# Performance work log

Measured on AMD Instinct MI355X. Metric: run time of the kernel, lower is better.

Reference implementation:

```python
import jax, jax.numpy as jnp
import numpy as np

B, S, D, H = 2, 2048, 1024, 16
HD = D // H
FF = 4 * D
EPS = 1e-5


def _ln(x, g, b):
    mu = jnp.mean(x, axis=-1, keepdims=True)
    var = jnp.var(x, axis=-1, keepdims=True)
    return (x - mu) * jax.lax.rsqrt(var + EPS) * g + b


def setup_inputs() -> dict:
    key = jax.random.key(0)
    ks = jax.random.split(key, 8)
    std = 0.02
    inp = {
        'x': jax.random.normal(ks[0], (B, S, D), jnp.float32),
        'mask': jnp.ones((B, S), jnp.int32),
        'Wq': jax.random.normal(ks[1], (D, D), jnp.float32) * std,
        'bq': jnp.zeros((D,), jnp.float32),
        'Wk': jax.random.normal(ks[2], (D, D), jnp.float32) * std,
        'bk': jnp.zeros((D,), jnp.float32),
        'Wv': jax.random.normal(ks[3], (D, D), jnp.float32) * std,
        'bv': jnp.zeros((D,), jnp.float32),
        'Wo': jax.random.normal(ks[4], (D, D), jnp.float32) * std,
        'bo': jnp.zeros((D,), jnp.float32),
        'W1': jax.random.normal(ks[5], (D, FF), jnp.float32) * std,
        'b1': jnp.zeros((FF,), jnp.float32),
        'W2': jax.random.normal(ks[6], (FF, D), jnp.float32) * std,
        'b2': jnp.zeros((D,), jnp.float32),
        'g1': jnp.ones((D,), jnp.float32),
        'be1': jnp.zeros((D,), jnp.float32),
        'g2': jnp.ones((D,), jnp.float32),
        'be2': jnp.zeros((D,), jnp.float32),
    }
    return inp


def reference(x, mask, Wq, bq, Wk, bk, Wv, bv, Wo, bo, W1, b1, W2, b2, g1, be1, g2, be2):
    # multi-head attention (dropout in eval mode => identity)
    q = (x @ Wq + bq).reshape(B, S, H, HD).transpose(0, 2, 1, 3)  # [B,H,S,HD]
    k = (x @ Wk + bk).reshape(B, S, H, HD).transpose(0, 2, 1, 3)
    v = (x @ Wv + bv).reshape(B, S, H, HD).transpose(0, 2, 1, 3)
    scores = jnp.einsum('bhqd,bhkd->bhqk', q, k) / jnp.sqrt(jnp.float32(HD))
    m = mask[:, None, None, :]  # [B,1,1,S] broadcast over queries
    scores = jnp.where(m == 0, jnp.float32(-1e9), scores)
    attn = jax.nn.softmax(scores, axis=-1)
    ao = jnp.einsum('bhqk,bhkd->bhqd', attn, v).transpose(0, 2, 1, 3).reshape(B, S, D)
    attn_out = ao @ Wo + bo
    x1 = _ln(x + attn_out, g1, be1)
    ffn = jax.nn.relu(x1 @ W1 + b1) @ W2 + b2
    return _ln(x1 + ffn, g2, be2)
```

## Files before the change

### kernel.cpp

```cpp
#include <hip/hip_runtime.h>
#include <stdint.h>
#include <stddef.h>

#define B_ 2
#define S_ 2048
#define D_ 1024
#define H_ 16
#define HD_ 64
#define FF_ 4096

typedef unsigned short u16;
typedef __attribute__((ext_vector_type(8))) short bf16x8;
typedef __attribute__((ext_vector_type(4))) float f32x4;

__device__ __forceinline__ u16 f2bf(float f) {
  unsigned u = __float_as_uint(f);
  u += 0x7fffu + ((u >> 16) & 1u);
  return (u16)(u >> 16);
}

__device__ __forceinline__ f32x4 mfma16(bf16x8 a, bf16x8 b, f32x4 c) {
  return __builtin_amdgcn_mfma_f32_16x16x32_bf16(a, b, c, 0, 0, 0);
}

__device__ __forceinline__ void gload16(const void* g, void* l) {
  __builtin_amdgcn_global_load_lds(
      (const __attribute__((address_space(1))) void*)g,
      (__attribute__((address_space(3))) void*)l, 16, 0, 0);
}

__device__ __forceinline__ void swizzle_mn(int& mt, int& nt) {
  int gm = gridDim.x;
  if ((gm & 7) == 0) {
    int bid = blockIdx.y * gm + blockIdx.x;
    int mper = gm >> 3;
    int xcd = bid & 7, idx = bid >> 3;
    mt = xcd * mper + (idx % mper);
    nt = idx / mper;
  } else {
    mt = blockIdx.x;
    nt = blockIdx.y;
  }
}

__global__ __launch_bounds__(256) void cvt_kernel(const float* __restrict__ src,
                                                  u16* __restrict__ dst, int n) {
  int i = (blockIdx.x * 256 + threadIdx.x) * 4;
  if (i >= n) return;
  float4 v = *(const float4*)(src + i);
  ushort4 o = { f2bf(v.x), f2bf(v.y), f2bf(v.z), f2bf(v.w) };
  *(ushort4*)(dst + i) = o;
}

__global__ __launch_bounds__(256) void transpose_cvt_kernel(
    const float* __restrict__ W, u16* __restrict__ WT, int K, int N) {
  __shared__ u16 t[32][33];
  int k0 = blockIdx.x * 32;
  int n0 = blockIdx.y * 32;
  int tid = threadIdx.x;
  int r = tid >> 3;
  int c = (tid & 7) << 2;
  float4 v = *(const float4*)(W + (size_t)(k0 + r) * N + n0 + c);
  t[r][c + 0] = f2bf(v.x); t[r][c + 1] = f2bf(v.y);
  t[r][c + 2] = f2bf(v.z); t[r][c + 3] = f2bf(v.w);
  __syncthreads();
  ushort4 o;
  o.x = t[c + 0][r]; o.y = t[c + 1][r]; o.z = t[c + 2][r]; o.w = t[c + 3][r];
  *(ushort4*)(WT + (size_t)(n0 + r) * K + k0 + c) = o;
}

__global__ __launch_bounds__(256) void gemm_bt_relu(
    const u16* __restrict__ A, const u16* __restrict__ BT,
    const float* __restrict__ bias, u16* __restrict__ outp,
    int M, int N, int K) {
  __shared__ __align__(16) u16 As[128 * 32];
  __shared__ __align__(16) u16 Bs[128 * 32];
  int tid = threadIdx.x;
  int lane = tid & 63;
  int wave = tid >> 6;
  int quad = lane >> 4;
  int l16 = lane & 15;
  int mt, nt;
  swizzle_mn(mt, nt);
  int m0 = mt * 128;
  int n0 = nt * 128;
  int wm = (wave >> 1) * 64;
  int wn = (wave & 1) * 64;

  f32x4 zero = {0.f, 0.f, 0.f, 0.f};
  f32x4 acc[4][4];
#pragma unroll
  for (int i = 0; i < 4; i++)
#pragma unroll
    for (int j = 0; j < 4; j++) acc[i][j] = zero;

  int c0 = tid, c1 = tid + 256;
  const u16* ga0 = A + (size_t)(m0 + (c0 >> 2)) * K + (c0 & 3) * 8;
  const u16* ga1 = A + (size_t)(m0 + (c1 >> 2)) * K + (c1 & 3) * 8;
  const u16* gb0 = BT + (size_t)(n0 + (c0 >> 2)) * K + (c0 & 3) * 8;
  const u16* gb1 = BT + (size_t)(n0 + (c1 >> 2)) * K + (c1 & 3) * 8;

  for (int k0 = 0; k0 < K; k0 += 32) {
    gload16(ga0 + k0, &As[c0 * 8]);
    gload16(ga1 + k0, &As[c1 * 8]);
    gload16(gb0 + k0, &Bs[c0 * 8]);
    gload16(gb1 + k0, &Bs[c1 * 8]);
    __syncthreads();
    bf16x8 af[4], bfr[4];
#pragma unroll
    for (int i = 0; i < 4; i++)
      af[i] = *(const bf16x8*)&As[(wm + i * 16 + l16) * 32 + quad * 8];
#pragma unroll
    for (int j = 0; j < 4; j++)
      bfr[j] = *(const bf16x8*)&Bs[(wn + j * 16 + l16) * 32 + quad * 8];
#pragma unroll
    for (int i = 0; i < 4; i++)
#pragma unroll
      for (int j = 0; j < 4; j++)
        acc[i][j] = mfma16(af[i], bfr[j], acc[i][j]);
    __syncthreads();
  }

#pragma unroll
  for (int j = 0; j < 4; j++) {
    int gcol = n0 + wn + j * 16 + l16;
    float bv = bias[gcol];
#pragma unroll
    for (int i = 0; i < 4; i++) {
#pragma unroll
      for (int r = 0; r < 4; r++) {
        int grow = m0 + wm + i * 16 + quad * 4 + r;
        float val = acc[i][j][r] + bv;
        outp[(size_t)grow * N + gcol] = f2bf(val > 0.f ? val : 0.f);
      }
    }
  }
}

__global__ __launch_bounds__(256) void gemm_bt_sk2(
    const u16* __restrict__ A, const u16* __restrict__ BT,
    const float* __restrict__ bias, float* __restrict__ outp,
    int M, int N, int K, int Kc) {
  __shared__ __align__(16) u16 As[128 * 32];
  __shared__ __align__(16) u16 Bs[128 * 32];
  int tid = threadIdx.x;
  int lane = tid & 63;
  int wave = tid >> 6;
  int quad = lane >> 4;
  int l16 = lane & 15;
  int mt, nt;
  swizzle_mn(mt, nt);
  int m0 = mt * 128;
  int n0 = nt * 128;
  int kb = blockIdx.z * Kc;
  int wm = (wave >> 1) * 64;
  int wn = (wave & 1) * 64;

  f32x4 zero = {0.f, 0.f, 0.f, 0.f};
  f32x4 acc[4][4];
#pragma unroll
  for (int i = 0; i < 4; i++)
#pragma unroll
    for (int j = 0; j < 4; j++) acc[i][j] = zero;

  int c0 = tid, c1 = tid + 256;
  const u16* ga0 = A + (size_t)(m0 + (c0 >> 2)) * K + (c0 & 3) * 8 + kb;
  const u16* ga1 = A + (size_t)(m0 + (c1 >> 2)) * K + (c1 & 3) * 8 + kb;
  const u16* gb0 = BT + (size_t)(n0 + (c0 >> 2)) * K + (c0 & 3) * 8 + kb;
  const u16* gb1 = BT + (size_t)(n0 + (c1 >> 2)) * K + (c1 & 3) * 8 + kb;

  for (int k0 = 0; k0 < Kc; k0 += 32) {
    gload16(ga0 + k0, &As[c0 * 8]);
    gload16(ga1 + k0, &As[c1 * 8]);
    gload16(gb0 + k0, &Bs[c0 * 8]);
    gload16(gb1 + k0, &Bs[c1 * 8]);
    __syncthreads();
    bf16x8 af[4], bfr[4];
#pragma unroll
    for (int i = 0; i < 4; i++)
      af[i] = *(const bf16x8*)&As[(wm + i * 16 + l16) * 32 + quad * 8];
#pragma unroll
    for (int j = 0; j < 4; j++)
      bfr[j] = *(const bf16x8*)&Bs[(wn + j * 16 + l16) * 32 + quad * 8];
#pragma unroll
    for (int i = 0; i < 4; i++)
#pragma unroll
      for (int j = 0; j < 4; j++)
        acc[i][j] = mfma16(af[i], bfr[j], acc[i][j]);
    __syncthreads();
  }

  float* outz = outp + (size_t)blockIdx.z * M * N;
  float biasmul = (blockIdx.z == 0) ? 1.f : 0.f;
#pragma unroll
  for (int j = 0; j < 4; j++) {
    int gcol = n0 + wn + j * 16 + l16;
    float bv = bias[gcol] * biasmul;
#pragma unroll
    for (int i = 0; i < 4; i++) {
#pragma unroll
      for (int r = 0; r < 4; r++) {
        int grow = m0 + wm + i * 16 + quad * 4 + r;
        outz[(size_t)grow * N + gcol] = acc[i][j][r] + bv;
      }
    }
  }
}

__global__ __launch_bounds__(256) void gemm_qkv(
    const u16* __restrict__ A, const u16* __restrict__ BT,
    const float* __restrict__ bq, const float* __restrict__ bk,
    const float* __restrict__ bvp,
    u16* __restrict__ qb, u16* __restrict__ kb, u16* __restrict__ vb) {
  const int K = 1024;
  __shared__ __align__(16) u16 As[128 * 32];
  __shared__ __align__(16) u16 Bs[128 * 32];
  int tid = threadIdx.x;
  int lane = tid & 63;
  int wave = tid >> 6;
  int quad = lane >> 4;
  int l16 = lane & 15;
  int mt, nt;
  swizzle_mn(mt, nt);
  int m0 = mt * 128;
  int n0 = nt * 128;
  int wm = (wave >> 1) * 64;
  int wn = (wave & 1) * 64;

  f32x4 zero = {0.f, 0.f, 0.f, 0.f};
  f32x4 acc[4][4];
#pragma unroll
  for (int i = 0; i < 4; i++)
#pragma unroll
    for (int j = 0; j < 4; j++) acc[i][j] = zero;

  int c0 = tid, c1 = tid + 256;
  const u16* ga0 = A + (size_t)(m0 + (c0 >> 2)) * K + (c0 & 3) * 8;
  const u16* ga1 = A + (size_t)(m0 + (c1 >> 2)) * K + (c1 & 3) * 8;
  const u16* gb0 = BT + (size_t)(n0 + (c0 >> 2)) * K + (c0 & 3) * 8;
  const u16* gb1 = BT + (size_t)(n0 + (c1 >> 2)) * K + (c1 & 3) * 8;

  for (int k0 = 0; k0 < K; k0 += 32) {
    gload16(ga0 + k0, &As[c0 * 8]);
    gload16(ga1 + k0, &As[c1 * 8]);
    gload16(gb0 + k0, &Bs[c0 * 8]);
    gload16(gb1 + k0, &Bs[c1 * 8]);
    __syncthreads();
    bf16x8 af[4], bfr[4];
#pragma unroll
    for (int i = 0; i < 4; i++)
      af[i] = *(const bf16x8*)&As[(wm + i * 16 + l16) * 32 + quad * 8];
#pragma unroll
    for (int j = 0; j < 4; j++)
      bfr[j] = *(const bf16x8*)&Bs[(wn + j * 16 + l16) * 32 + quad * 8];
#pragma unroll
    for (int i = 0; i < 4; i++)
#pragma unroll
      for (int j = 0; j < 4; j++)
        acc[i][j] = mfma16(af[i], bfr[j], acc[i][j]);
    __syncthreads();
  }

  int region = n0 >> 10;
  const float* bias = region == 0 ? bq : (region == 1 ? bk : bvp);
  u16* outp = region == 0 ? qb : (region == 1 ? kb : vb);
  float scale = region == 0 ? 0.125f * 1.4426950408889634f : 1.f;

#pragma unroll
  for (int j = 0; j < 4; j++) {
    int gcol = (n0 & 1023) + wn + j * 16 + l16;
    float bv = bias[gcol];
    int h = gcol >> 6, hd = gcol & 63;
#pragma unroll
    for (int i = 0; i < 4; i++) {
#pragma unroll
      for (int r = 0; r < 4; r++) {
        int grow = m0 + wm + i * 16 + quad * 4 + r;
        float val = (acc[i][j][r] + bv) * scale;
        int b = grow >> 11, s = grow & 2047;
        if (region < 2) {
          outp[(((size_t)(b * H_ + h)) * S_ + s) * HD_ + hd] = f2bf(val);
        } else {
          outp[(((size_t)(b * H_ + h)) * HD_ + hd) * S_ + s] = f2bf(val);
        }
      }
    }
  }
}

__global__ __launch_bounds__(256, 4) void attn_kernel(
    const u16* __restrict__ q, const u16* __restrict__ k,
    const u16* __restrict__ vt, const int* __restrict__ mask,
    u16* __restrict__ ao) {
  __shared__ __align__(16) u16 Ks[64 * 72];
  __shared__ __align__(16) u16 Vs[64 * 72];
  __shared__ __align__(16) u16 Ps[4][32 * 72];
  int tid = threadIdx.x;
  int lane = tid & 63;
  int wave = tid >> 6;
  int quad = lane >> 4;
  int l16 = lane & 15;
  int bh = blockIdx.y;
  int b = bh >> 4;
  int h = bh & 15;
  int qrow0 = blockIdx.x * 128 + wave * 32;

  const u16* qh = q + (size_t)bh * S_ * HD_;
  const u16* kh = k + (size_t)bh * S_ * HD_;
  const u16* vh = vt + (size_t)bh * HD_ * S_;

  bf16x8 qfA0 = *(const bf16x8*)(qh + (size_t)(qrow0 + l16) * HD_ + quad * 8);
  bf16x8 qfA1 = *(const bf16x8*)(qh + (size_t)(qrow0 + l16) * HD_ + 32 + quad * 8);
  bf16x8 qfB0 = *(const bf16x8*)(qh + (size_t)(qrow0 + 16 + l16) * HD_ + quad * 8);
  bf16x8 qfB1 = *(const bf16x8*)(qh + (size_t)(qrow0 + 16 + l16) * HD_ + 32 + quad * 8);

  int sr = tid >> 3, sc = tid & 7;
  const u16* kg0 = kh + sr * HD_ + sc * 8;
  const u16* kg1 = kh + (sr + 32) * HD_ + sc * 8;
  const u16* vg0 = vh + (size_t)sr * S_ + sc * 8;
  const u16* vg1 = vh + (size_t)(sr + 32) * S_ + sc * 8;
  int kr0 = (sr & 1) * 16 + (sr >> 1);
  int ko0 = kr0 * 72 + sc * 8;
  int ko1 = (32 + kr0) * 72 + sc * 8;
  int vo0 = sr * 72 + sc * 8;
  int vo1 = (sr + 32) * 72 + sc * 8;
  const int* mrow = mask + b * S_ + 2 * l16;

  float l_pA[4] = {0.f, 0.f, 0.f, 0.f};
  float l_pB[4] = {0.f, 0.f, 0.f, 0.f};
  f32x4 zero = {0.f, 0.f, 0.f, 0.f};
  f32x4 o_accA[4], o_accB[4];
#pragma unroll
  for (int c = 0; c < 4; c++) { o_accA[c] = zero; o_accB[c] = zero; }

  u16* pw = &Ps[wave][0];

  for (int kt = 0; kt < S_; kt += 64) {
    bf16x8 kv0 = *(const bf16x8*)(kg0 + (size_t)kt * HD_);
    bf16x8 kv1 = *(const bf16x8*)(kg1 + (size_t)kt * HD_);
    bf16x8 vv0 = *(const bf16x8*)(vg0 + kt);
    bf16x8 vv1 = *(const bf16x8*)(vg1 + kt);
    int2 mk0 = *(const int2*)(mrow + kt);
    int2 mk1 = *(const int2*)(mrow + kt + 32);

    __syncthreads();
    *(bf16x8*)&Ks[ko0] = kv0;
    *(bf16x8*)&Ks[ko1] = kv1;
    *(bf16x8*)&Vs[vo0] = vv0;
    *(bf16x8*)&Vs[vo1] = vv1;
    __syncthreads();

#pragma unroll
    for (int g = 0; g < 2; g++) {
      int2 mk = g == 0 ? mk0 : mk1;
      int rowe = (g * 32 + l16) * 72;
      int rowo = (g * 32 + 16 + l16) * 72;
      bf16x8 e0 = *(const bf16x8*)&Ks[rowe + quad * 8];
      bf16x8 e1 = *(const bf16x8*)&Ks[rowe + 32 + quad * 8];
      bf16x8 o0 = *(const bf16x8*)&Ks[rowo + quad * 8];
      bf16x8 o1 = *(const bf16x8*)&Ks[rowo + 32 + quad * 8];
      f32x4 seA = mfma16(qfA1, e1, mfma16(qfA0, e0, zero));
      f32x4 soA = mfma16(qfA1, o1, mfma16(qfA0, o0, zero));
      f32x4 seB = mfma16(qfB1, e1, mfma16(qfB0, e0, zero));
      f32x4 soB = mfma16(qfB1, o1, mfma16(qfB0, o0, zero));
#pragma unroll
      for (int r = 0; r < 4; r++) {
        float pA0 = mk.x ? exp2f(seA[r]) : 0.f;
        float pA1 = mk.y ? exp2f(soA[r]) : 0.f;
        float pB0 = mk.x ? exp2f(seB[r]) : 0.f;
        float pB1 = mk.y ? exp2f(soB[r]) : 0.f;
        l_pA[r] += pA0 + pA1;
        l_pB[r] += pB0 + pB1;
        unsigned pkA = __builtin_amdgcn_perm(__float_as_uint(pA1),
                                             __float_as_uint(pA0), 0x07060302u);
        unsigned pkB = __builtin_amdgcn_perm(__float_as_uint(pB1),
                                             __float_as_uint(pB0), 0x07060302u);
        *(unsigned*)&pw[(quad * 4 + r) * 72 + g * 32 + 2 * l16] = pkA;
        *(unsigned*)&pw[(16 + quad * 4 + r) * 72 + g * 32 + 2 * l16] = pkB;
      }
    }
    bf16x8 pfA0 = *(const bf16x8*)&pw[l16 * 72 + quad * 8];
    bf16x8 pfA1 = *(const bf16x8*)&pw[l16 * 72 + 32 + quad * 8];
    bf16x8 pfB0 = *(const bf16x8*)&pw[(16 + l16) * 72 + quad * 8];
    bf16x8 pfB1 = *(const bf16x8*)&pw[(16 + l16) * 72 + 32 + quad * 8];
#pragma unroll
    for (int c = 0; c < 4; c++) {
      bf16x8 vf0 = *(const bf16x8*)&Vs[(c * 16 + l16) * 72 + quad * 8];
      bf16x8 vf1 = *(const bf16x8*)&Vs[(c * 16 + l16) * 72 + 32 + quad * 8];
      o_accA[c] = mfma16(pfA1, vf1, mfma16(pfA0, vf0, o_accA[c]));
      o_accB[c] = mfma16(pfB1, vf1, mfma16(pfB0, vf0, o_accB[c]));
    }
  }

#pragma unroll
  for (int r = 0; r < 4; r++) {
    float sA = l_pA[r], sB = l_pB[r];
#pragma unroll
    for (int off = 1; off < 16; off <<= 1) {
      sA += __shfl_xor(sA, off);
      sB += __shfl_xor(sB, off);
    }
    float invA = 1.f / sA, invB = 1.f / sB;
    int srowA = qrow0 + quad * 4 + r;
    int srowB = qrow0 + 16 + quad * 4 + r;
#pragma unroll
    for (int c = 0; c < 4; c++) {
      ao[((size_t)(b * S_ + srowA)) * D_ + h * HD_ + c * 16 + l16] =
          f2bf(o_accA[c][r] * invA);
      ao[((size_t)(b * S_ + srowB)) * D_ + h * HD_ + c * 16 + l16] =
          f2bf(o_accB[c][r] * invB);
    }
  }
}

__global__ __launch_bounds__(256) void ln_kernel(
    const float* __restrict__ xa, const float* __restrict__ add0,
    const float* __restrict__ add1,
    const float* __restrict__ g, const float* __restrict__ be,
    float* __restrict__ outf, u16* __restrict__ outb) {
  int row = blockIdx.x;
  int tid = threadIdx.x;
  int lane = tid & 63;
  int wv = tid >> 6;
  const float4 a = *(const float4*)(xa + (size_t)row * D_ + tid * 4);
  const float4 c = *(const float4*)(add0 + (size_t)row * D_ + tid * 4);
  const float4 d = *(const float4*)(add1 + (size_t)row * D_ + tid * 4);
  float v0 = a.x + c.x + d.x, v1 = a.y + c.y + d.y;
  float v2 = a.z + c.z + d.z, v3 = a.w + c.w + d.w;
  float s = v0 + v1 + v2 + v3;
  float sq = v0 * v0 + v1 * v1 + v2 * v2 + v3 * v3;
#pragma unroll
  for (int off = 1; off < 64; off <<= 1) {
    s += __shfl_xor(s, off);
    sq += __shfl_xor(sq, off);
  }
  __shared__ float red[8];
  if (lane == 0) { red[wv] = s; red[4 + wv] = sq; }
  __syncthreads();
  s = red[0] + red[1] + red[2] + red[3];
  sq = red[4] + red[5] + red[6] + red[7];
  float mean = s * (1.f / D_);
  float var = sq * (1.f / D_) - mean * mean;
  float rstd = rsqrtf(var + 1e-5f);
  const float4 gv = *(const float4*)(g + tid * 4);
  const float4 bv = *(const float4*)(be + tid * 4);
  float y0 = (v0 - mean) * rstd * gv.x + bv.x;
  float y1 = (v1 - mean) * rstd * gv.y + bv.y;
  float y2 = (v2 - mean) * rstd * gv.z + bv.z;
  float y3 = (v3 - mean) * rstd * gv.w + bv.w;
  float4 o = {y0, y1, y2, y3};
  *(float4*)(outf + (size_t)row * D_ + tid * 4) = o;
  if (outb) {
    ushort4 ob = {f2bf(y0), f2bf(y1), f2bf(y2), f2bf(y3)};
    *(ushort4*)(outb + (size_t)row * D_ + tid * 4) = ob;
  }
}

extern "C" void kernel_launch(void* const* d_in, const int* in_sizes, int n_in,
                              void* d_out, int out_size, void* d_ws, size_t ws_size,
                              hipStream_t stream) {
  const float* x = (const float*)d_in[0];
  const int* mask = (const int*)d_in[1];
  const float* Wq = (const float*)d_in[2];
  const float* bq = (const float*)d_in[3];
  const float* Wk = (const float*)d_in[4];
  const float* bk = (const float*)d_in[5];
  const float* Wv = (const float*)d_in[6];
  const float* bv = (const float*)d_in[7];
  const float* Wo = (const float*)d_in[8];
  const float* bo = (const float*)d_in[9];
  const float* W1 = (const float*)d_in[10];
  const float* b1 = (const float*)d_in[11];
  const float* W2 = (const float*)d_in[12];
  const float* b2 = (const float*)d_in[13];
  const float* g1 = (const float*)d_in[14];
  const float* be1 = (const float*)d_in[15];
  const float* g2 = (const float*)d_in[16];
  const float* be2 = (const float*)d_in[17];

  const size_t MB = 1ull << 20;
  char* ws = (char*)d_ws;
  u16* wTq = (u16*)(ws + 0 * MB);
  u16* wTk = (u16*)(ws + 2 * MB);
  u16* wTv = (u16*)(ws + 4 * MB);
  u16* wTo = (u16*)(ws + 6 * MB);
  u16* w1T = (u16*)(ws + 8 * MB);
  u16* w2T = (u16*)(ws + 16 * MB);
  u16* xb  = (u16*)(ws + 24 * MB);
  u16* qb  = (u16*)(ws + 32 * MB);
  u16* kb  = (u16*)(ws + 40 * MB);
  u16* vb  = (u16*)(ws + 48 * MB);
  u16* ao  = (u16*)(ws + 56 * MB);
  float* proj = (float*)(ws + 64 * MB);
  float* x1f  = (float*)(ws + 24 * MB);
  u16*   x1b  = (u16*)(ws + 40 * MB);
  u16*   h1   = (u16*)(ws + 96 * MB);
  float* ffn2 = (float*)(ws + 48 * MB);

  cvt_kernel<<<dim3((B_ * S_ * D_) / 1024), dim3(256), 0, stream>>>(x, xb, B_ * S_ * D_);
  transpose_cvt_kernel<<<dim3(32, 32), dim3(256), 0, stream>>>(Wq, wTq, D_, D_);
  transpose_cvt_kernel<<<dim3(32, 32), dim3(256), 0, stream>>>(Wk, wTk, D_, D_);
  transpose_cvt_kernel<<<dim3(32, 32), dim3(256), 0, stream>>>(Wv, wTv, D_, D_);
  transpose_cvt_kernel<<<dim3(32, 32), dim3(256), 0, stream>>>(Wo, wTo, D_, D_);
  transpose_cvt_kernel<<<dim3(32, 128), dim3(256), 0, stream>>>(W1, w1T, D_, FF_);
  transpose_cvt_kernel<<<dim3(128, 32), dim3(256), 0, stream>>>(W2, w2T, FF_, D_);

  gemm_qkv<<<dim3(32, 24), dim3(256), 0, stream>>>(xb, wTq, bq, bk, bv, qb, kb, vb);

  attn_kernel<<<dim3(S_ / 128, B_ * H_), dim3(256), 0, stream>>>(qb, kb, vb, mask, ao);

  gemm_bt_sk2<<<dim3(32, 8, 2), dim3(256), 0, stream>>>(ao, wTo, bo, proj, 4096, 1024, 1024, 512);

  ln_kernel<<<dim3(4096), dim3(256), 0, stream>>>(
      x, proj, proj + (size_t)4096 * 1024, g1, be1, x1f, x1b);

  gemm_bt_relu<<<dim3(32, 32), dim3(256), 0, stream>>>(x1b, w1T, b1, h1, 4096, 4096, 1024);

  gemm_bt_sk2<<<dim3(32, 8, 2), dim3(256), 0, stream>>>(h1, w2T, b2, ffn2, 4096, 1024, 4096, 2048);

  ln_kernel<<<dim3(4096), dim3(256), 0, stream>>>(
      x1f, ffn2, ffn2 + (size_t)4096 * 1024, g2, be2, (float*)d_out, (u16*)nullptr);
}
```

Baseline: 408.2 us.

## Double-buffer attention K/V tiles, merge weight transposes, split-K by four for FFN2

The attention kernel now double-buffers K/V tiles in shared memory and prefetches the next tile into registers, so one barrier per iteration is dropped. Occupancy hint goes from 4 to 2 blocks per CU. The four square weight transposes are merged into one launch. The second FFN GEMM is split four ways along K instead of two, and a new LayerNorm kernel sums the four partials. This trades more partial-sum traffic and more shared memory for parallelism and overlap.

```diff
diff --git a/kernel.cpp b/kernel.cpp
--- a/kernel.cpp
+++ b/kernel.cpp
@@ -69,6 +69,29 @@
   *(ushort4*)(WT + (size_t)(n0 + r) * K + k0 + c) = o;
 }
 
+__global__ __launch_bounds__(256) void transpose_cvt4_kernel(
+    const float* __restrict__ s0, const float* __restrict__ s1,
+    const float* __restrict__ s2, const float* __restrict__ s3,
+    u16* __restrict__ d0, u16* __restrict__ d1,
+    u16* __restrict__ d2, u16* __restrict__ d3) {
+  __shared__ u16 t[32][33];
+  int z = blockIdx.z;
+  const float* W = z == 0 ? s0 : (z == 1 ? s1 : (z == 2 ? s2 : s3));
+  u16* WT = z == 0 ? d0 : (z == 1 ? d1 : (z == 2 ? d2 : d3));
+  int k0 = blockIdx.x * 32;
+  int n0 = blockIdx.y * 32;
+  int tid = threadIdx.x;
+  int r = tid >> 3;
+  int c = (tid & 7) << 2;
+  float4 v = *(const float4*)(W + (size_t)(k0 + r) * D_ + n0 + c);
+  t[r][c + 0] = f2bf(v.x); t[r][c + 1] = f2bf(v.y);
+  t[r][c + 2] = f2bf(v.z); t[r][c + 3] = f2bf(v.w);
+  __syncthreads();
+  ushort4 o;
+  o.x = t[c + 0][r]; o.y = t[c + 1][r]; o.z = t[c + 2][r]; o.w = t[c + 3][r];
+  *(ushort4*)(WT + (size_t)(n0 + r) * D_ + k0 + c) = o;
+}
+
 __global__ __launch_bounds__(256) void gemm_bt_relu(
     const u16* __restrict__ A, const u16* __restrict__ BT,
     const float* __restrict__ bias, u16* __restrict__ outp,
@@ -137,9 +160,11 @@
   }
 }
 
-__global__ __launch_bounds__(256) void gemm_bt_sk2(
+__global__ __launch_bounds__(256) void gemm_bt_sk4(
     const u16* __restrict__ A, const u16* __restrict__ BT,
-    const float* __restrict__ bias, float* __restrict__ outp,
+    const float* __restrict__ bias,
+    float* __restrict__ o0, float* __restrict__ o1,
+    float* __restrict__ o2, float* __restrict__ o3,
     int M, int N, int K, int Kc) {
   __shared__ __align__(16) u16 As[128 * 32];
   __shared__ __align__(16) u16 Bs[128 * 32];
@@ -152,7 +177,8 @@
   swizzle_mn(mt, nt);
   int m0 = mt * 128;
   int n0 = nt * 128;
-  int kb = blockIdx.z * Kc;
+  int z = blockIdx.z;
+  int kb = z * Kc;
   int wm = (wave >> 1) * 64;
   int wn = (wave & 1) * 64;
 
@@ -190,8 +216,8 @@
     __syncthreads();
   }
 
-  float* outz = outp + (size_t)blockIdx.z * M * N;
-  float biasmul = (blockIdx.z == 0) ? 1.f : 0.f;
+  float* outz = z == 0 ? o0 : (z == 1 ? o1 : (z == 2 ? o2 : o3));
+  float biasmul = (z == 0) ? 1.f : 0.f;
 #pragma unroll
   for (int j = 0; j < 4; j++) {
     int gcol = n0 + wn + j * 16 + l16;
@@ -288,12 +314,12 @@
   }
 }
 
-__global__ __launch_bounds__(256, 4) void attn_kernel(
+__global__ __launch_bounds__(256, 2) void attn_kernel(
     const u16* __restrict__ q, const u16* __restrict__ k,
     const u16* __restrict__ vt, const int* __restrict__ mask,
     u16* __restrict__ ao) {
-  __shared__ __align__(16) u16 Ks[64 * 72];
-  __shared__ __align__(16) u16 Vs[64 * 72];
+  __shared__ __align__(16) u16 Ks[2][64 * 72];
+  __shared__ __align__(16) u16 Vs[2][64 * 72];
   __shared__ __align__(16) u16 Ps[4][32 * 72];
   int tid = threadIdx.x;
   int lane = tid & 63;
@@ -335,30 +361,49 @@
 
   u16* pw = &Ps[wave][0];
 
+  bf16x8 kv0 = *(const bf16x8*)(kg0);
+  bf16x8 kv1 = *(const bf16x8*)(kg1);
+  bf16x8 vv0 = *(const bf16x8*)(vg0);
+  bf16x8 vv1 = *(const bf16x8*)(vg1);
+  *(bf16x8*)&Ks[0][ko0] = kv0;
+  *(bf16x8*)&Ks[0][ko1] = kv1;
+  *(bf16x8*)&Vs[0][vo0] = vv0;
+  *(bf16x8*)&Vs[0][vo1] = vv1;
+  kv0 = *(const bf16x8*)(kg0 + (size_t)64 * HD_);
+  kv1 = *(const bf16x8*)(kg1 + (size_t)64 * HD_);
+  vv0 = *(const bf16x8*)(vg0 + 64);
+  vv1 = *(const bf16x8*)(vg1 + 64);
+
+  int cur = 0;
   for (int kt = 0; kt < S_; kt += 64) {
-    bf16x8 kv0 = *(const bf16x8*)(kg0 + (size_t)kt * HD_);
-    bf16x8 kv1 = *(const bf16x8*)(kg1 + (size_t)kt * HD_);
-    bf16x8 vv0 = *(const bf16x8*)(vg0 + kt);
-    bf16x8 vv1 = *(const bf16x8*)(vg1 + kt);
     int2 mk0 = *(const int2*)(mrow + kt);
     int2 mk1 = *(const int2*)(mrow + kt + 32);
 
     __syncthreads();
-    *(bf16x8*)&Ks[ko0] = kv0;
-    *(bf16x8*)&Ks[ko1] = kv1;
-    *(bf16x8*)&Vs[vo0] = vv0;
-    *(bf16x8*)&Vs[vo1] = vv1;
-    __syncthreads();
-
+    if (kt + 64 < S_) {
+      int alt = cur ^ 1;
+      *(bf16x8*)&Ks[alt][ko0] = kv0;
+      *(bf16x8*)&Ks[alt][ko1] = kv1;
+      *(bf16x8*)&Vs[alt][vo0] = vv0;
+      *(bf16x8*)&Vs[alt][vo1] = vv1;
+      int nk = (kt + 128) & (S_ - 1);
+      kv0 = *(const bf16x8*)(kg0 + (size_t)nk * HD_);
+      kv1 = *(const bf16x8*)(kg1 + (size_t)nk * HD_);
+      vv0 = *(const bf16x8*)(vg0 + nk);
+      vv1 = *(const bf16x8*)(vg1 + nk);
+    }
+
+    const u16* ksb = &Ks[cur][0];
+    const u16* vsb = &Vs[cur][0];
 #pragma unroll
     for (int g = 0; g < 2; g++) {
       int2 mk = g == 0 ? mk0 : mk1;
       int rowe = (g * 32 + l16) * 72;
       int rowo = (g * 32 + 16 + l16) * 72;
-      bf16x8 e0 = *(const bf16x8*)&Ks[rowe + quad * 8];
-      bf16x8 e1 = *(const bf16x8*)&Ks[rowe + 32 + quad * 8];
-      bf16x8 o0 = *(const bf16x8*)&Ks[rowo + quad * 8];
-      bf16x8 o1 = *(const bf16x8*)&Ks[rowo + 32 + quad * 8];
+      bf16x8 e0 = *(const bf16x8*)&ksb[rowe + quad * 8];
+      bf16x8 e1 = *(const bf16x8*)&ksb[rowe + 32 + quad * 8];
+      bf16x8 o0 = *(const bf16x8*)&ksb[rowo + quad * 8];
+      bf16x8 o1 = *(const bf16x8*)&ksb[rowo + 32 + quad * 8];
       f32x4 seA = mfma16(qfA1, e1, mfma16(qfA0, e0, zero));
       f32x4 soA = mfma16(qfA1, o1, mfma16(qfA0, o0, zero));
       f32x4 seB = mfma16(qfB1, e1, mfma16(qfB0, e0, zero));
@@ -385,11 +430,12 @@
     bf16x8 pfB1 = *(const bf16x8*)&pw[(16 + l16) * 72 + 32 + quad * 8];
 #pragma unroll
     for (int c = 0; c < 4; c++) {
-      bf16x8 vf0 = *(const bf16x8*)&Vs[(c * 16 + l16) * 72 + quad * 8];
-      bf16x8 vf1 = *(const bf16x8*)&Vs[(c * 16 + l16) * 72 + 32 + quad * 8];
+      bf16x8 vf0 = *(const bf16x8*)&vsb[(c * 16 + l16) * 72 + quad * 8];
+      bf16x8 vf1 = *(const bf16x8*)&vsb[(c * 16 + l16) * 72 + 32 + quad * 8];
       o_accA[c] = mfma16(pfA1, vf1, mfma16(pfA0, vf0, o_accA[c]));
       o_accB[c] = mfma16(pfB1, vf1, mfma16(pfB0, vf0, o_accB[c]));
     }
+    cur ^= 1;
   }
 
 #pragma unroll
@@ -453,6 +499,55 @@
   if (outb) {
     ushort4 ob = {f2bf(y0), f2bf(y1), f2bf(y2), f2bf(y3)};
     *(ushort4*)(outb + (size_t)row * D_ + tid * 4) = ob;
+  }
+}
+
+__global__ __launch_bounds__(256) void ln4_kernel(
+    const float* __restrict__ xa,
+    const float* __restrict__ a0, const float* __restrict__ a1,
+    const float* __restrict__ a2, const float* __restrict__ a3,
+    const float* __restrict__ g, const float* __restrict__ be,
+    float* __restrict__ outf, u16* __restrict__ outb) {
+  int row = blockIdx.x;
+  int tid = threadIdx.x;
+  int lane = tid & 63;
+  int wv = tid >> 6;
+  size_t off0 = (size_t)row * D_ + tid * 4;
+  const float4 a = *(const float4*)(xa + off0);
+  const float4 c0 = *(const float4*)(a0 + off0);
+  const float4 c1 = *(const float4*)(a1 + off0);
+  const float4 c2 = *(const float4*)(a2 + off0);
+  const float4 c3 = *(const float4*)(a3 + off0);
+  float v0 = a.x + (c0.x + c1.x) + (c2.x + c3.x);
+  float v1 = a.y + (c0.y + c1.y) + (c2.y + c3.y);
+  float v2 = a.z + (c0.z + c1.z) + (c2.z + c3.z);
+  float v3 = a.w + (c0.w + c1.w) + (c2.w + c3.w);
+  float s = v0 + v1 + v2 + v3;
+  float sq = v0 * v0 + v1 * v1 + v2 * v2 + v3 * v3;
+#pragma unroll
+  for (int off = 1; off < 64; off <<= 1) {
+    s += __shfl_xor(s, off);
+    sq += __shfl_xor(sq, off);
+  }
+  __shared__ float red[8];
+  if (lane == 0) { red[wv] = s; red[4 + wv] = sq; }
+  __syncthreads();
+  s = red[0] + red[1] + red[2] + red[3];
+  sq = red[4] + red[5] + red[6] + red[7];
+  float mean = s * (1.f / D_);
+  float var = sq * (1.f / D_) - mean * mean;
+  float rstd = rsqrtf(var + 1e-5f);
+  const float4 gv = *(const float4*)(g + tid * 4);
+  const float4 bv = *(const float4*)(be + tid * 4);
+  float y0 = (v0 - mean) * rstd * gv.x + bv.x;
+  float y1 = (v1 - mean) * rstd * gv.y + bv.y;
+  float y2 = (v2 - mean) * rstd * gv.z + bv.z;
+  float y3 = (v3 - mean) * rstd * gv.w + bv.w;
+  float4 o = {y0, y1, y2, y3};
+  *(float4*)(outf + off0) = o;
+  if (outb) {
+    ushort4 ob = {f2bf(y0), f2bf(y1), f2bf(y2), f2bf(y3)};
+    *(ushort4*)(outb + off0) = ob;
   }
 }
 
@@ -491,17 +586,19 @@
   u16* kb  = (u16*)(ws + 40 * MB);
   u16* vb  = (u16*)(ws + 48 * MB);
   u16* ao  = (u16*)(ws + 56 * MB);
-  float* proj = (float*)(ws + 64 * MB);
-  float* x1f  = (float*)(ws + 24 * MB);
-  u16*   x1b  = (u16*)(ws + 40 * MB);
-  u16*   h1   = (u16*)(ws + 96 * MB);
-  float* ffn2 = (float*)(ws + 48 * MB);
+  float* p0 = (float*)(ws + 64 * MB);
+  float* p1 = (float*)(ws + 80 * MB);
+  float* x1f = (float*)(ws + 24 * MB);
+  u16*   x1b = (u16*)(ws + 40 * MB);
+  u16*   h1  = (u16*)(ws + 48 * MB);
+  float* f0 = (float*)(ws + 80 * MB);
+  float* f1 = (float*)(ws + 96 * MB);
+  float* f2 = (float*)(ws + 112 * MB);
+  float* f3 = (float*)(ws + 0 * MB);
 
   cvt_kernel<<<dim3((B_ * S_ * D_) / 1024), dim3(256), 0, stream>>>(x, xb, B_ * S_ * D_);
-  transpose_cvt_kernel<<<dim3(32, 32), dim3(256), 0, stream>>>(Wq, wTq, D_, D_);
-  transpose_cvt_kernel<<<dim3(32, 32), dim3(256), 0, stream>>>(Wk, wTk, D_, D_);
-  transpose_cvt_kernel<<<dim3(32, 32), dim3(256), 0, stream>>>(Wv, wTv, D_, D_);
-  transpose_cvt_kernel<<<dim3(32, 32), dim3(256), 0, stream>>>(Wo, wTo, D_, D_);
+  transpose_cvt4_kernel<<<dim3(32, 32, 4), dim3(256), 0, stream>>>(
+      Wq, Wk, Wv, Wo, wTq, wTk, wTv, wTo);
   transpose_cvt_kernel<<<dim3(32, 128), dim3(256), 0, stream>>>(W1, w1T, D_, FF_);
   transpose_cvt_kernel<<<dim3(128, 32), dim3(256), 0, stream>>>(W2, w2T, FF_, D_);
 
@@ -509,15 +606,16 @@
 
   attn_kernel<<<dim3(S_ / 128, B_ * H_), dim3(256), 0, stream>>>(qb, kb, vb, mask, ao);
 
-  gemm_bt_sk2<<<dim3(32, 8, 2), dim3(256), 0, stream>>>(ao, wTo, bo, proj, 4096, 1024, 1024, 512);
-
-  ln_kernel<<<dim3(4096), dim3(256), 0, stream>>>(
-      x, proj, proj + (size_t)4096 * 1024, g1, be1, x1f, x1b);
+  gemm_bt_sk4<<<dim3(32, 8, 2), dim3(256), 0, stream>>>(
+      ao, wTo, bo, p0, p1, p0, p0, 4096, 1024, 1024, 512);
+
+  ln_kernel<<<dim3(4096), dim3(256), 0, stream>>>(x, p0, p1, g1, be1, x1f, x1b);
 
   gemm_bt_relu<<<dim3(32, 32), dim3(256), 0, stream>>>(x1b, w1T, b1, h1, 4096, 4096, 1024);
 
-  gemm_bt_sk2<<<dim3(32, 8, 2), dim3(256), 0, stream>>>(h1, w2T, b2, ffn2, 4096, 1024, 4096, 2048);
-
-  ln_kernel<<<dim3(4096), dim3(256), 0, stream>>>(
-      x1f, ffn2, ffn2 + (size_t)4096 * 1024, g2, be2, (float*)d_out, (u16*)nullptr);
-}
+  gemm_bt_sk4<<<dim3(32, 8, 4), dim3(256), 0, stream>>>(
+      h1, w2T, b2, f0, f1, f2, f3, 4096, 1024, 4096, 1024);
+
+  ln4_kernel<<<dim3(4096), dim3(256), 0, stream>>>(
+      x1f, f0, f1, f2, f3, g2, be2, (float*)d_out, (u16*)nullptr);
+}
```

Result: no change. 406.1 us (-0.5%).
